# Performance work log

Measured on AMD Instinct MI355X. Metric: run time of the kernel, lower is better.

The kernel has to match this reference:

```python
import jax, jax.numpy as jnp
import numpy as np

N_NODES = 100000
N_EDGES = 1600000
N_CONCEPTS = 500000
D = 128  # concept_dim = graph_hidden_dim = graph_output_dim


def setup_inputs() -> dict:
    key = jax.random.key(0)
    ks = jax.random.split(key, 10)
    cncpt_ids = jax.random.randint(ks[0], (N_NODES,), 0, N_CONCEPTS)
    src = jax.random.randint(ks[1], (N_EDGES,), 0, N_NODES)
    dst = jax.random.randint(ks[2], (N_EDGES,), 0, N_NODES)
    emb_table = jax.random.normal(ks[3], (N_CONCEPTS, D), dtype=jnp.float32)
    W1 = jax.random.normal(ks[4], (D, D), dtype=jnp.float32) * 0.05
    b1 = jax.random.normal(ks[5], (D,), dtype=jnp.float32) * 0.05
    W2 = jax.random.normal(ks[6], (D, D), dtype=jnp.float32) * 0.05
    b2 = jax.random.normal(ks[7], (D,), dtype=jnp.float32) * 0.05
    Wout = jax.random.normal(ks[8], (1, D), dtype=jnp.float32) * 0.05
    bout = jax.random.normal(ks[9], (1,), dtype=jnp.float32) * 0.05
    return {"cncpt_ids": cncpt_ids, "src": src, "dst": dst,
            "emb_table": emb_table, "W1": W1, "b1": b1,
            "W2": W2, "b2": b2, "Wout": Wout, "bout": bout}


def _gcn_layer(h, src, dst, W, b, n_nodes):
    # DGL update_all(copy_src, sum): gather messages from src, sum into dst
    agg = jax.ops.segment_sum(h[src], dst, num_segments=n_nodes)  # [N, d_in]
    return jax.nn.relu(agg @ W.T + b)  # NodeApplyModule: Linear + ReLU


def reference(cncpt_ids, src, dst, emb_table, W1, b1, W2, b2, Wout, bout):
    n_nodes = cncpt_ids.shape[0]
    h = emb_table[cncpt_ids]                       # [N, D] concept embeddings
    h = _gcn_layer(h, src, dst, W1, b1, n_nodes)   # gcn1
    h = _gcn_layer(h, src, dst, W2, b2, n_nodes)   # gcn2
    x = h[None]                                    # torch.stack([h]) -> [1, N, D]
    logits = jax.nn.sigmoid(x @ Wout.T + bout)     # hidden2output -> [1, N, 1]
    return logits
```

## Files before the change

kernel.cpp:

```cpp
#include <hip/hip_runtime.h>
#include <math.h>

#define D 128
#define SCAN_B 256

typedef __attribute__((ext_vector_type(8))) short bfrag;
typedef __attribute__((ext_vector_type(4))) float ffrag;

__device__ inline unsigned short f2bf(float f) {
    unsigned u = __float_as_uint(f);
    u += 0x7FFF + ((u >> 16) & 1);
    return (unsigned short)(u >> 16);
}
__device__ inline float bf2f(unsigned short h) {
    return __uint_as_float(((unsigned)h) << 16);
}
__device__ inline unsigned pack_bf2(float a, float b) {
    return ((unsigned)f2bf(a)) | (((unsigned)f2bf(b)) << 16);
}

__global__ void setup1_kernel(const float* __restrict__ W1,
                              const float* __restrict__ W2,
                              unsigned short* __restrict__ hi1,
                              unsigned short* __restrict__ lo1,
                              unsigned short* __restrict__ hi2,
                              unsigned short* __restrict__ lo2,
                              int* __restrict__ deg, int np1, int nblk_w) {
    if ((int)blockIdx.x < nblk_w) {
        int i = blockIdx.x * blockDim.x + threadIdx.x;
        if (i < D * D) {
            float f1 = W1[i];
            unsigned short h1 = f2bf(f1);
            hi1[i] = h1;
            lo1[i] = f2bf(f1 - bf2f(h1));
            float f2 = W2[i];
            unsigned short h2 = f2bf(f2);
            hi2[i] = h2;
            lo2[i] = f2bf(f2 - bf2f(h2));
        }
    } else {
        int i = ((int)blockIdx.x - nblk_w) * blockDim.x + threadIdx.x;
        if (i < np1) deg[i] = 0;
    }
}

__global__ void setup2_kernel(const float* __restrict__ emb,
                              const int* __restrict__ ids,
                              uint4* __restrict__ h4,
                              const int* __restrict__ dst,
                              int* __restrict__ deg,
                              int n_nodes, int n_edges, int nblk_g) {
    if ((int)blockIdx.x < nblk_g) {
        int idx = blockIdx.x * blockDim.x + threadIdx.x;
        int total = n_nodes * 16;
        if (idx >= total) return;
        int node = idx >> 4;
        int c = idx & 15;
        size_t cid = (size_t)ids[node];
        const float4* s = (const float4*)(emb + cid * D) + c * 2;
        float4 v0 = s[0];
        float4 v1 = s[1];
        uint4 p;
        p.x = pack_bf2(v0.x, v0.y);
        p.y = pack_bf2(v0.z, v0.w);
        p.z = pack_bf2(v1.x, v1.y);
        p.w = pack_bf2(v1.z, v1.w);
        h4[(size_t)node * 16 + c] = p;
    } else {
        int e = ((int)blockIdx.x - nblk_g) * blockDim.x + threadIdx.x;
        if (e < n_edges) atomicAdd(&deg[dst[e]], 1);
    }
}

__global__ __launch_bounds__(SCAN_B) void scan_block_kernel(
        const int* __restrict__ deg, int* __restrict__ row_ptr,
        int* __restrict__ blocksums, int n) {
    __shared__ int s[SCAN_B];
    int i = blockIdx.x * SCAN_B + threadIdx.x;
    int v = (i < n) ? deg[i] : 0;
    s[threadIdx.x] = v;
    __syncthreads();
    #pragma unroll
    for (int off = 1; off < SCAN_B; off <<= 1) {
        int t = (threadIdx.x >= off) ? s[threadIdx.x - off] : 0;
        __syncthreads();
        s[threadIdx.x] += t;
        __syncthreads();
    }
    if (i < n) row_ptr[i] = s[threadIdx.x] - v;
    if (threadIdx.x == SCAN_B - 1) blocksums[blockIdx.x] = s[SCAN_B - 1];
}

__global__ __launch_bounds__(512) void scan_sums_kernel(int* __restrict__ blocksums,
                                                        int nb) {
    __shared__ int s[512];
    int v = (threadIdx.x < nb) ? blocksums[threadIdx.x] : 0;
    s[threadIdx.x] = v;
    __syncthreads();
    #pragma unroll
    for (int off = 1; off < 512; off <<= 1) {
        int t = (threadIdx.x >= off) ? s[threadIdx.x - off] : 0;
        __syncthreads();
        s[threadIdx.x] += t;
        __syncthreads();
    }
    if (threadIdx.x < nb) blocksums[threadIdx.x] = s[threadIdx.x] - v;
}

__global__ void add_offsets_kernel(int* __restrict__ row_ptr,
                                   const int* __restrict__ blocksums,
                                   int* __restrict__ cursor, int n, int n_nodes) {
    int i = blockIdx.x * blockDim.x + threadIdx.x;
    if (i >= n) return;
    int rp = row_ptr[i] + blocksums[i / SCAN_B];
    row_ptr[i] = rp;
    if (i < n_nodes) cursor[i] = rp;
}

__global__ void csr_fill_kernel(const int* __restrict__ src,
                                const int* __restrict__ dst,
                                int* __restrict__ cursor,
                                int* __restrict__ esrc, int n_edges) {
    int e = blockIdx.x * blockDim.x + threadIdx.x;
    if (e >= n_edges) return;
    int pos = atomicAdd(&cursor[dst[e]], 1);
    esrc[pos] = src[e];
}

#define ACC8(u) do { \
    a0 += __uint_as_float((u).x << 16); a1 += __uint_as_float((u).x & 0xffff0000u); \
    a2 += __uint_as_float((u).y << 16); a3 += __uint_as_float((u).y & 0xffff0000u); \
    a4 += __uint_as_float((u).z << 16); a5 += __uint_as_float((u).z & 0xffff0000u); \
    a6 += __uint_as_float((u).w << 16); a7 += __uint_as_float((u).w & 0xffff0000u); \
} while (0)

__global__ __launch_bounds__(256) void agg_kernel(
        const uint4* __restrict__ h4, const int* __restrict__ row_ptr,
        const int* __restrict__ esrc, uint4* __restrict__ agg4, int n_nodes) {
    int node = blockIdx.x * 4 + (threadIdx.x >> 6);
    int lane = threadIdx.x & 63;
    if (node >= n_nodes) return;
    const int c = lane & 15;
    const int g = lane >> 4;
    int beg = row_ptr[node], end = row_ptr[node + 1];
    int deg = end - beg;

    int myidx = 0;
    if (lane < deg) myidx = esrc[beg + lane];

    float a0 = 0.f, a1 = 0.f, a2 = 0.f, a3 = 0.f;
    float a4 = 0.f, a5 = 0.f, a6 = 0.f, a7 = 0.f;

    int nfast = deg < 64 ? deg : 64;
    for (int base = 0; base < nfast; base += 16) {
        int p0 = base + g;
        int s0 = __shfl(myidx, p0, 64);
        int s1 = __shfl(myidx, p0 + 4, 64);
        int s2 = __shfl(myidx, p0 + 8, 64);
        int s3 = __shfl(myidx, p0 + 12, 64);
        bool v0 = p0 < nfast;
        bool v1 = (p0 + 4) < nfast;
        bool v2 = (p0 + 8) < nfast;
        bool v3 = (p0 + 12) < nfast;
        uint4 u0, u1, u2, u3;
        if (v0) u0 = h4[(size_t)s0 * 16 + c];
        if (v1) u1 = h4[(size_t)s1 * 16 + c];
        if (v2) u2 = h4[(size_t)s2 * 16 + c];
        if (v3) u3 = h4[(size_t)s3 * 16 + c];
        if (v0) ACC8(u0);
        if (v1) ACC8(u1);
        if (v2) ACC8(u2);
        if (v3) ACC8(u3);
    }
    for (int i = beg + 64 + g; i < end; i += 4) {
        uint4 u = h4[(size_t)esrc[i] * 16 + c];
        ACC8(u);
    }

    a0 += __shfl_xor(a0, 16, 64); a0 += __shfl_xor(a0, 32, 64);
    a1 += __shfl_xor(a1, 16, 64); a1 += __shfl_xor(a1, 32, 64);
    a2 += __shfl_xor(a2, 16, 64); a2 += __shfl_xor(a2, 32, 64);
    a3 += __shfl_xor(a3, 16, 64); a3 += __shfl_xor(a3, 32, 64);
    a4 += __shfl_xor(a4, 16, 64); a4 += __shfl_xor(a4, 32, 64);
    a5 += __shfl_xor(a5, 16, 64); a5 += __shfl_xor(a5, 32, 64);
    a6 += __shfl_xor(a6, 16, 64); a6 += __shfl_xor(a6, 32, 64);
    a7 += __shfl_xor(a7, 16, 64); a7 += __shfl_xor(a7, 32, 64);

    if (g == 0) {
        uint4 r;
        r.x = pack_bf2(a0, a1);
        r.y = pack_bf2(a2, a3);
        r.z = pack_bf2(a4, a5);
        r.w = pack_bf2(a6, a7);
        agg4[(size_t)node * 16 + c] = r;
    }
}

__global__ __launch_bounds__(256) void linear_mfma_kernel(
        const unsigned short* __restrict__ x,
        const unsigned short* __restrict__ Whi,
        const unsigned short* __restrict__ Wlo,
        const float* __restrict__ b,
        unsigned short* __restrict__ y,
        const float* __restrict__ wout,
        const float* __restrict__ bout,
        float* __restrict__ outp,
        int n_nodes, int fuse_out) {
    __shared__ __align__(16) unsigned short sW[2][D][136];

    {
        const uint4* Wh4 = (const uint4*)Whi;
        const uint4* Wl4 = (const uint4*)Wlo;
        #pragma unroll
        for (int j = 0; j < 8; ++j) {
            int ch = (int)threadIdx.x + j * 256;
            int row = ch >> 4, k8 = ch & 15;
            *(uint4*)&sW[0][row][k8 * 8] = Wh4[ch];
            *(uint4*)&sW[1][row][k8 * 8] = Wl4[ch];
        }
    }
    __syncthreads();

    const int lane = threadIdx.x & 63;
    const int col  = lane & 15;
    const int quad = lane >> 4;
    const int wave = blockIdx.x * 4 + (threadIdx.x >> 6);
    const int nwaves = gridDim.x * 4;
    const int ngroups = (n_nodes + 15) >> 4;

    float bvals[8], wvals[8];
    #pragma unroll
    for (int nt = 0; nt < 8; ++nt) {
        bvals[nt] = b[nt * 16 + col];
        wvals[nt] = fuse_out ? wout[nt * 16 + col] : 0.f;
    }
    const float bout0 = fuse_out ? bout[0] : 0.f;

    for (int g = wave; g < ngroups; g += nwaves) {
        int node = g * 16 + col;
        int nload = node < n_nodes ? node : (n_nodes - 1);

        bfrag a[4];
        #pragma unroll
        for (int kt = 0; kt < 4; ++kt)
            a[kt] = *(const bfrag*)(x + (size_t)nload * D + kt * 32 + quad * 8);

        float part0 = 0.f, part1 = 0.f, part2 = 0.f, part3 = 0.f;

        #pragma unroll
        for (int nt = 0; nt < 8; ++nt) {
            ffrag c = {0.f, 0.f, 0.f, 0.f};
            #pragma unroll
            for (int kt = 0; kt < 4; ++kt) {
                bfrag bh = *(const bfrag*)&sW[0][nt * 16 + col][kt * 32 + quad * 8];
                bfrag bl = *(const bfrag*)&sW[1][nt * 16 + col][kt * 32 + quad * 8];
                c = __builtin_amdgcn_mfma_f32_16x16x32_bf16(a[kt], bh, c, 0, 0, 0);
                c = __builtin_amdgcn_mfma_f32_16x16x32_bf16(a[kt], bl, c, 0, 0, 0);
            }
            if (fuse_out) {
                part0 += fmaxf(c[0] + bvals[nt], 0.f) * wvals[nt];
                part1 += fmaxf(c[1] + bvals[nt], 0.f) * wvals[nt];
                part2 += fmaxf(c[2] + bvals[nt], 0.f) * wvals[nt];
                part3 += fmaxf(c[3] + bvals[nt], 0.f) * wvals[nt];
            } else {
                #pragma unroll
                for (int r = 0; r < 4; ++r) {
                    int onode = g * 16 + quad * 4 + r;
                    if (onode < n_nodes)
                        y[(size_t)onode * D + nt * 16 + col] =
                            f2bf(fmaxf(c[r] + bvals[nt], 0.f));
                }
            }
        }

        if (fuse_out) {
            float part[4] = {part0, part1, part2, part3};
            #pragma unroll
            for (int r = 0; r < 4; ++r) {
                float s = part[r];
                s += __shfl_xor(s, 1, 64);
                s += __shfl_xor(s, 2, 64);
                s += __shfl_xor(s, 4, 64);
                s += __shfl_xor(s, 8, 64);
                int onode = g * 16 + quad * 4 + r;
                if (col == 0 && onode < n_nodes)
                    outp[onode] = 1.0f / (1.0f + expf(-(s + bout0)));
            }
        }
    }
}

extern "C" void kernel_launch(void* const* d_in, const int* in_sizes, int n_in,
                              void* d_out, int out_size, void* d_ws, size_t ws_size,
                              hipStream_t stream) {
    const int*   cncpt_ids = (const int*)d_in[0];
    const int*   src       = (const int*)d_in[1];
    const int*   dst       = (const int*)d_in[2];
    const float* emb       = (const float*)d_in[3];
    const float* W1        = (const float*)d_in[4];
    const float* b1        = (const float*)d_in[5];
    const float* W2        = (const float*)d_in[6];
    const float* b2        = (const float*)d_in[7];
    const float* Wout      = (const float*)d_in[8];
    const float* bout      = (const float*)d_in[9];
    float* out = (float*)d_out;

    const int n_nodes = in_sizes[0];
    const int n_edges = in_sizes[1];

    unsigned short* bufA = (unsigned short*)d_ws;
    unsigned short* bufB = bufA + (size_t)n_nodes * D;
    int*   deg      = (int*)(bufB + (size_t)n_nodes * D);
    int*   row_ptr  = deg + (n_nodes + 1);
    int*   cursor   = row_ptr + (n_nodes + 1);
    int*   blocksums= cursor + n_nodes;
    int*   esrc     = blocksums + 512;
    size_t walign   = ((size_t)(esrc + n_edges) + 15) & ~(size_t)15;
    unsigned short* W1hi = (unsigned short*)walign;
    unsigned short* W1lo = W1hi + D * D;
    unsigned short* W2hi = W1lo + D * D;
    unsigned short* W2lo = W2hi + D * D;

    const int np1 = n_nodes + 1;
    const int nb_scan = (np1 + SCAN_B - 1) / SCAN_B;

    const int nblk_w = (D * D + 255) / 256;
    const int nblk_z = (np1 + 255) / 256;
    setup1_kernel<<<nblk_w + nblk_z, 256, 0, stream>>>(
        W1, W2, W1hi, W1lo, W2hi, W2lo, deg, np1, nblk_w);

    const int nblk_g = (n_nodes * 16 + 255) / 256;
    const int nblk_d = (n_edges + 255) / 256;
    setup2_kernel<<<nblk_g + nblk_d, 256, 0, stream>>>(
        emb, cncpt_ids, (uint4*)bufA, dst, deg, n_nodes, n_edges, nblk_g);

    scan_block_kernel<<<nb_scan, SCAN_B, 0, stream>>>(deg, row_ptr, blocksums, np1);
    scan_sums_kernel<<<1, 512, 0, stream>>>(blocksums, nb_scan);
    add_offsets_kernel<<<(np1 + 255) / 256, 256, 0, stream>>>(
        row_ptr, blocksums, cursor, np1, n_nodes);
    csr_fill_kernel<<<nblk_d, 256, 0, stream>>>(src, dst, cursor, esrc, n_edges);

    const int agg_grid = (n_nodes + 3) / 4;
    const int ngroups = (n_nodes + 15) / 16;
    const int lin_grid = (ngroups + 7) / 8;

    agg_kernel<<<agg_grid, 256, 0, stream>>>(
        (const uint4*)bufA, row_ptr, esrc, (uint4*)bufB, n_nodes);
    linear_mfma_kernel<<<lin_grid, 256, 0, stream>>>(
        bufB, W1hi, W1lo, b1, bufA, nullptr, nullptr, nullptr, n_nodes, 0);

    agg_kernel<<<agg_grid, 256, 0, stream>>>(
        (const uint4*)bufA, row_ptr, esrc, (uint4*)bufB, n_nodes);
    linear_mfma_kernel<<<lin_grid, 256, 0, stream>>>(
        bufB, W2hi, W2lo, b2, nullptr, Wout, bout, out, n_nodes, 1);
}
```

Before: 674.3 us.

## Replace CSR scan build with fixed-capacity per-node edge buckets

Measured after the change: 620.5 us. 1.09x faster.

```diff
diff --git a/kernel.cpp b/kernel.cpp
--- a/kernel.cpp
+++ b/kernel.cpp
@@ -2,7 +2,7 @@
 #include <math.h>
 
 #define D 128
-#define SCAN_B 256
+#define CAP 128
 
 typedef __attribute__((ext_vector_type(8))) short bfrag;
 typedef __attribute__((ext_vector_type(4))) float ffrag;
@@ -18,6 +18,13 @@
 __device__ inline unsigned pack_bf2(float a, float b) {
     return ((unsigned)f2bf(a)) | (((unsigned)f2bf(b)) << 16);
 }
+
+#define ACC8(u) do { \
+    a0 += __uint_as_float((u).x << 16); a1 += __uint_as_float((u).x & 0xffff0000u); \
+    a2 += __uint_as_float((u).y << 16); a3 += __uint_as_float((u).y & 0xffff0000u); \
+    a4 += __uint_as_float((u).z << 16); a5 += __uint_as_float((u).z & 0xffff0000u); \
+    a6 += __uint_as_float((u).w << 16); a7 += __uint_as_float((u).w & 0xffff0000u); \
+} while (0)
 
 __global__ void setup1_kernel(const float* __restrict__ W1,
                               const float* __restrict__ W2,
@@ -25,7 +32,7 @@
                               unsigned short* __restrict__ lo1,
                               unsigned short* __restrict__ hi2,
                               unsigned short* __restrict__ lo2,
-                              int* __restrict__ deg, int np1, int nblk_w) {
+                              int* __restrict__ cnt, int n_nodes, int nblk_w) {
     if ((int)blockIdx.x < nblk_w) {
         int i = blockIdx.x * blockDim.x + threadIdx.x;
         if (i < D * D) {
@@ -40,15 +47,17 @@
         }
     } else {
         int i = ((int)blockIdx.x - nblk_w) * blockDim.x + threadIdx.x;
-        if (i < np1) deg[i] = 0;
+        if (i < n_nodes) cnt[i] = 0;
     }
 }
 
 __global__ void setup2_kernel(const float* __restrict__ emb,
                               const int* __restrict__ ids,
                               uint4* __restrict__ h4,
+                              const int* __restrict__ src,
                               const int* __restrict__ dst,
-                              int* __restrict__ deg,
+                              int* __restrict__ cnt,
+                              int* __restrict__ bucket,
                               int n_nodes, int n_edges, int nblk_g) {
     if ((int)blockIdx.x < nblk_g) {
         int idx = blockIdx.x * blockDim.x + threadIdx.x;
@@ -68,113 +77,85 @@
         h4[(size_t)node * 16 + c] = p;
     } else {
         int e = ((int)blockIdx.x - nblk_g) * blockDim.x + threadIdx.x;
-        if (e < n_edges) atomicAdd(&deg[dst[e]], 1);
-    }
-}
-
-__global__ __launch_bounds__(SCAN_B) void scan_block_kernel(
-        const int* __restrict__ deg, int* __restrict__ row_ptr,
-        int* __restrict__ blocksums, int n) {
-    __shared__ int s[SCAN_B];
-    int i = blockIdx.x * SCAN_B + threadIdx.x;
-    int v = (i < n) ? deg[i] : 0;
-    s[threadIdx.x] = v;
-    __syncthreads();
-    #pragma unroll
-    for (int off = 1; off < SCAN_B; off <<= 1) {
-        int t = (threadIdx.x >= off) ? s[threadIdx.x - off] : 0;
-        __syncthreads();
-        s[threadIdx.x] += t;
-        __syncthreads();
-    }
-    if (i < n) row_ptr[i] = s[threadIdx.x] - v;
-    if (threadIdx.x == SCAN_B - 1) blocksums[blockIdx.x] = s[SCAN_B - 1];
-}
-
-__global__ __launch_bounds__(512) void scan_sums_kernel(int* __restrict__ blocksums,
-                                                        int nb) {
-    __shared__ int s[512];
-    int v = (threadIdx.x < nb) ? blocksums[threadIdx.x] : 0;
-    s[threadIdx.x] = v;
-    __syncthreads();
-    #pragma unroll
-    for (int off = 1; off < 512; off <<= 1) {
-        int t = (threadIdx.x >= off) ? s[threadIdx.x - off] : 0;
-        __syncthreads();
-        s[threadIdx.x] += t;
-        __syncthreads();
-    }
-    if (threadIdx.x < nb) blocksums[threadIdx.x] = s[threadIdx.x] - v;
-}
-
-__global__ void add_offsets_kernel(int* __restrict__ row_ptr,
-                                   const int* __restrict__ blocksums,
-                                   int* __restrict__ cursor, int n, int n_nodes) {
-    int i = blockIdx.x * blockDim.x + threadIdx.x;
-    if (i >= n) return;
-    int rp = row_ptr[i] + blocksums[i / SCAN_B];
-    row_ptr[i] = rp;
-    if (i < n_nodes) cursor[i] = rp;
-}
-
-__global__ void csr_fill_kernel(const int* __restrict__ src,
-                                const int* __restrict__ dst,
-                                int* __restrict__ cursor,
-                                int* __restrict__ esrc, int n_edges) {
-    int e = blockIdx.x * blockDim.x + threadIdx.x;
-    if (e >= n_edges) return;
-    int pos = atomicAdd(&cursor[dst[e]], 1);
-    esrc[pos] = src[e];
-}
-
-#define ACC8(u) do { \
-    a0 += __uint_as_float((u).x << 16); a1 += __uint_as_float((u).x & 0xffff0000u); \
-    a2 += __uint_as_float((u).y << 16); a3 += __uint_as_float((u).y & 0xffff0000u); \
-    a4 += __uint_as_float((u).z << 16); a5 += __uint_as_float((u).z & 0xffff0000u); \
-    a6 += __uint_as_float((u).w << 16); a7 += __uint_as_float((u).w & 0xffff0000u); \
-} while (0)
+        if (e >= n_edges) return;
+        int d = dst[e];
+        int pos = atomicAdd(&cnt[d], 1);
+        if (pos < CAP) bucket[(size_t)d * CAP + pos] = src[e];
+    }
+}
 
 __global__ __launch_bounds__(256) void agg_kernel(
-        const uint4* __restrict__ h4, const int* __restrict__ row_ptr,
-        const int* __restrict__ esrc, uint4* __restrict__ agg4, int n_nodes) {
+        const uint4* __restrict__ h4,
+        const int* __restrict__ cnt,
+        const int* __restrict__ bucket,
+        const int* __restrict__ src,
+        const int* __restrict__ dst,
+        uint4* __restrict__ agg4,
+        int n_nodes, int n_edges) {
     int node = blockIdx.x * 4 + (threadIdx.x >> 6);
     int lane = threadIdx.x & 63;
     if (node >= n_nodes) return;
     const int c = lane & 15;
     const int g = lane >> 4;
-    int beg = row_ptr[node], end = row_ptr[node + 1];
-    int deg = end - beg;
-
-    int myidx = 0;
-    if (lane < deg) myidx = esrc[beg + lane];
+    int deg = cnt[node];
 
     float a0 = 0.f, a1 = 0.f, a2 = 0.f, a3 = 0.f;
     float a4 = 0.f, a5 = 0.f, a6 = 0.f, a7 = 0.f;
 
-    int nfast = deg < 64 ? deg : 64;
-    for (int base = 0; base < nfast; base += 16) {
-        int p0 = base + g;
-        int s0 = __shfl(myidx, p0, 64);
-        int s1 = __shfl(myidx, p0 + 4, 64);
-        int s2 = __shfl(myidx, p0 + 8, 64);
-        int s3 = __shfl(myidx, p0 + 12, 64);
-        bool v0 = p0 < nfast;
-        bool v1 = (p0 + 4) < nfast;
-        bool v2 = (p0 + 8) < nfast;
-        bool v3 = (p0 + 12) < nfast;
-        uint4 u0, u1, u2, u3;
-        if (v0) u0 = h4[(size_t)s0 * 16 + c];
-        if (v1) u1 = h4[(size_t)s1 * 16 + c];
-        if (v2) u2 = h4[(size_t)s2 * 16 + c];
-        if (v3) u3 = h4[(size_t)s3 * 16 + c];
-        if (v0) ACC8(u0);
-        if (v1) ACC8(u1);
-        if (v2) ACC8(u2);
-        if (v3) ACC8(u3);
-    }
-    for (int i = beg + 64 + g; i < end; i += 4) {
-        uint4 u = h4[(size_t)esrc[i] * 16 + c];
-        ACC8(u);
+    if (deg <= CAP) {
+        const int beg = node * CAP;
+        int myidx = 0;
+        if (lane < deg) myidx = bucket[beg + lane];
+
+        int nfast = deg < 64 ? deg : 64;
+        for (int base = 0; base < nfast; base += 32) {
+            int p0 = base + g;
+            int p4 = p0 + 16;
+            int s0 = __shfl(myidx, p0, 64);
+            int s1 = __shfl(myidx, p0 + 4, 64);
+            int s2 = __shfl(myidx, p0 + 8, 64);
+            int s3 = __shfl(myidx, p0 + 12, 64);
+            int s4i = __shfl(myidx, p4, 64);
+            int s5 = __shfl(myidx, p4 + 4, 64);
+            int s6 = __shfl(myidx, p4 + 8, 64);
+            int s7 = __shfl(myidx, p4 + 12, 64);
+            bool v0 = p0 < nfast;
+            bool v1 = (p0 + 4) < nfast;
+            bool v2 = (p0 + 8) < nfast;
+            bool v3 = (p0 + 12) < nfast;
+            bool v4 = p4 < nfast;
+            bool v5 = (p4 + 4) < nfast;
+            bool v6 = (p4 + 8) < nfast;
+            bool v7 = (p4 + 12) < nfast;
+            uint4 u0, u1, u2, u3, u4, u5, u6, u7;
+            if (v0) u0 = h4[(size_t)s0 * 16 + c];
+            if (v1) u1 = h4[(size_t)s1 * 16 + c];
+            if (v2) u2 = h4[(size_t)s2 * 16 + c];
+            if (v3) u3 = h4[(size_t)s3 * 16 + c];
+            if (v4) u4 = h4[(size_t)s4i * 16 + c];
+            if (v5) u5 = h4[(size_t)s5 * 16 + c];
+            if (v6) u6 = h4[(size_t)s6 * 16 + c];
+            if (v7) u7 = h4[(size_t)s7 * 16 + c];
+            if (v0) ACC8(u0);
+            if (v1) ACC8(u1);
+            if (v2) ACC8(u2);
+            if (v3) ACC8(u3);
+            if (v4) ACC8(u4);
+            if (v5) ACC8(u5);
+            if (v6) ACC8(u6);
+            if (v7) ACC8(u7);
+        }
+        for (int i = 64 + g; i < deg; i += 4) {
+            uint4 u = h4[(size_t)bucket[beg + i] * 16 + c];
+            ACC8(u);
+        }
+    } else {
+        for (int e = g; e < n_edges; e += 4) {
+            if (dst[e] == node) {
+                uint4 u = h4[(size_t)src[e] * 16 + c];
+                ACC8(u);
+            }
+        }
     }
 
     a0 += __shfl_xor(a0, 16, 64); a0 += __shfl_xor(a0, 32, 64);
@@ -290,6 +271,7 @@
     }
 }
 
+
 extern "C" void kernel_launch(void* const* d_in, const int* in_sizes, int n_in,
                               void* d_out, int out_size, void* d_ws, size_t ws_size,
                               hipStream_t stream) {
@@ -310,47 +292,38 @@
 
     unsigned short* bufA = (unsigned short*)d_ws;
     unsigned short* bufB = bufA + (size_t)n_nodes * D;
-    int*   deg      = (int*)(bufB + (size_t)n_nodes * D);
-    int*   row_ptr  = deg + (n_nodes + 1);
-    int*   cursor   = row_ptr + (n_nodes + 1);
-    int*   blocksums= cursor + n_nodes;
-    int*   esrc     = blocksums + 512;
-    size_t walign   = ((size_t)(esrc + n_edges) + 15) & ~(size_t)15;
+    int*   cnt    = (int*)(bufB + (size_t)n_nodes * D);
+    int*   bucket = cnt + n_nodes;
+    size_t walign = ((size_t)(bucket + (size_t)n_nodes * CAP) + 15) & ~(size_t)15;
     unsigned short* W1hi = (unsigned short*)walign;
     unsigned short* W1lo = W1hi + D * D;
     unsigned short* W2hi = W1lo + D * D;
     unsigned short* W2lo = W2hi + D * D;
 
-    const int np1 = n_nodes + 1;
-    const int nb_scan = (np1 + SCAN_B - 1) / SCAN_B;
-
     const int nblk_w = (D * D + 255) / 256;
-    const int nblk_z = (np1 + 255) / 256;
+    const int nblk_z = (n_nodes + 255) / 256;
     setup1_kernel<<<nblk_w + nblk_z, 256, 0, stream>>>(
-        W1, W2, W1hi, W1lo, W2hi, W2lo, deg, np1, nblk_w);
+        W1, W2, W1hi, W1lo, W2hi, W2lo, cnt, n_nodes, nblk_w);
 
     const int nblk_g = (n_nodes * 16 + 255) / 256;
     const int nblk_d = (n_edges + 255) / 256;
     setup2_kernel<<<nblk_g + nblk_d, 256, 0, stream>>>(
-        emb, cncpt_ids, (uint4*)bufA, dst, deg, n_nodes, n_edges, nblk_g);
-
-    scan_block_kernel<<<nb_scan, SCAN_B, 0, stream>>>(deg, row_ptr, blocksums, np1);
-    scan_sums_kernel<<<1, 512, 0, stream>>>(blocksums, nb_scan);
-    add_offsets_kernel<<<(np1 + 255) / 256, 256, 0, stream>>>(
-        row_ptr, blocksums, cursor, np1, n_nodes);
-    csr_fill_kernel<<<nblk_d, 256, 0, stream>>>(src, dst, cursor, esrc, n_edges);
+        emb, cncpt_ids, (uint4*)bufA, src, dst, cnt, bucket,
+        n_nodes, n_edges, nblk_g);
 
     const int agg_grid = (n_nodes + 3) / 4;
     const int ngroups = (n_nodes + 15) / 16;
     const int lin_grid = (ngroups + 7) / 8;
 
     agg_kernel<<<agg_grid, 256, 0, stream>>>(
-        (const uint4*)bufA, row_ptr, esrc, (uint4*)bufB, n_nodes);
+        (const uint4*)bufA, cnt, bucket, src, dst, (uint4*)bufB,
+        n_nodes, n_edges);
     linear_mfma_kernel<<<lin_grid, 256, 0, stream>>>(
         bufB, W1hi, W1lo, b1, bufA, nullptr, nullptr, nullptr, n_nodes, 0);
 
     agg_kernel<<<agg_grid, 256, 0, stream>>>(
-        (const uint4*)bufA, row_ptr, esrc, (uint4*)bufB, n_nodes);
+        (const uint4*)bufA, cnt, bucket, src, dst, (uint4*)bufB,
+        n_nodes, n_edges);
     linear_mfma_kernel<<<lin_grid, 256, 0, stream>>>(
         bufB, W2hi, W2lo, b2, nullptr, Wout, bout, out, n_nodes, 1);
 }
```
